# Kernel optimization log

Hardware: AMD Instinct MI355X
Metric: run time of the kernel (lower is better)

Reference implementation:

```python
import jax, jax.numpy as jnp
import numpy as np

NT, NS, NH = 1096, 2048, 16

def setup_inputs() -> dict:
    key = jax.random.key(0)
    ks = jax.random.split(key, 6)
    # precipitation (non-negative) and temperature (can be +/-)
    P = jax.random.uniform(ks[0], (NT, NS), dtype=jnp.float32) * 10.0
    T = jax.random.normal(ks[1], (NT, NS), dtype=jnp.float32) * 10.0
    w_i = jax.random.uniform(ks[2], (NH,), minval=-1.0, maxval=1.0, dtype=jnp.float32)
    w_o = jax.random.uniform(ks[3], (NH,), minval=-1.0, maxval=1.0, dtype=jnp.float32)
    w_l = jax.random.uniform(ks[4], (NH,), minval=-1.0, maxval=1.0, dtype=jnp.float32)  # LinearBucket.w
    w_s = jax.random.uniform(ks[5], (NH,), minval=-1.0, maxval=2.0, dtype=jnp.float32)  # SnowBucket.w
    return dict(P=P, T=T, w_i=w_i, w_o=w_o, w_l=w_l, w_s=w_s)


def reference(P, T, w_i, w_o, w_l, w_s):
    # Time-invariant gate factors (Dropout is identity in eval mode)
    melt_coef = jnp.exp(w_s) + 1.0          # [nh]
    gi = jax.nn.sigmoid(w_i)                # [nh] input gate
    gl = jax.nn.sigmoid(w_l)                # [nh] linear-bucket release fraction
    a = jax.nn.softmax(w_o)                 # [nh] output mixing weights

    ns = P.shape[1]
    nh = w_i.shape[0]
    s0 = jnp.zeros((ns, nh), P.dtype)
    h0 = jnp.zeros((ns, nh), P.dtype)

    def step(carry, pt):
        s, h = carry
        Pk, Tk = pt                          # [ns]
        # SnowBucket (nm=0: melt m = min(potential melt, snow store))
        sm = jax.nn.relu(Tk)[:, None] * melt_coef      # [ns, nh]
        m = jnp.minimum(sm, s)
        sn = s - m + jnp.where(Tk < 0, Pk, 0.0)[:, None]
        x = jnp.where(Tk > 0, Pk, 0.0)[:, None] + m
        # input gate + LinearBucket
        xin = x * gi
        q = (xin + h) * gl
        hn = h - q + xin
        Qk = jnp.sum(q * a, axis=1)                    # [ns]
        return (sn, hn), (Qk, hn, sn)

    _, (Q, H, S) = jax.lax.scan(step, (s0, h0), (P, T))
    return Q, H, S
```

## Files before the change

### kernel.cpp

```cpp
#include <hip/hip_runtime.h>


constexpr int NT  = 1096;
constexpr int NS  = 2048;
constexpr int NH  = 16;
constexpr int NSH = NS * NH;
constexpr int SG  = 4;
constexpr int NC  = 8;
constexpr int L   = NT / NC;
static_assert(NC * L == NT, "");
constexpr int BT  = NC * SG * NH;
constexpr int NXCD = 8;

__device__ __forceinline__ float sigm(float x) { return 1.0f / (1.0f + expf(-x)); }

__global__ __launch_bounds__(BT, 4) void waternet_fused(
    const float* __restrict__ P, const float* __restrict__ T,
    const float* __restrict__ w_i, const float* __restrict__ w_o,
    const float* __restrict__ w_l, const float* __restrict__ w_s,
    float* __restrict__ Q, float* __restrict__ H, float* __restrict__ S)
{
    __shared__ float2 PTs[SG][NT + 2];
    __shared__ float bufA[BT];
    __shared__ float bufB[BT];
    __shared__ float bufC[BT];

    const int nwg = NS / SG;
    const int cpx = nwg / NXCD;
    const int bid = (int)blockIdx.x;
    const int lbid = (bid % NXCD) * cpx + bid / NXCD;

    const int tid  = (int)threadIdx.x;
    const int hh   = tid & (NH - 1);
    const int sl   = (tid >> 4) & (SG - 1);
    const int c    = tid >> 6;
    const int site0 = lbid * SG;

    for (int e = tid; e < SG * NT; e += BT) {
        const int t  = e >> 2;
        const int s2 = e & 3;
        const float p  = P[(size_t)t * NS + site0 + s2];
        const float tt = T[(size_t)t * NS + site0 + s2];
        PTs[s2][t] = make_float2(p, tt);
    }

    const float mc = expf(w_s[hh]) + 1.0f;
    const float gi = sigm(w_i[hh]);
    const float gl = sigm(w_l[hh]);
    const float cl = 1.0f - gl;

    const int t0 = c * L;
    __syncthreads();

    float A = 0.0f, B = -1e38f;
    for (int i = 0; i < L; ++i) {
        const float2 pt = PTs[sl][t0 + i];
        const float tpos = fmaxf(pt.y, 0.0f);
        const float pnn  = (pt.y < 0.0f) ? pt.x : 0.0f;
        const float at   = pnn - tpos * mc;
        A += at;
        B = fmaxf(B + at, pnn);
    }
    bufA[tid] = A;
    bufB[tid] = B;
    __syncthreads();

    if (tid < SG * NH) {
        float s = 0.0f;
        #pragma unroll
        for (int k = 0; k < NC; ++k) {
            const int idx = k * (SG * NH) + tid;
            bufC[idx] = s;
            s = fmaxf(s + bufA[idx], bufB[idx]);
        }
    }
    __syncthreads();

    float s = bufC[tid];
    float hp = 0.0f;
    {
        float* Sp = S + (size_t)t0 * NSH + (size_t)site0 * NH + sl * NH + hh;
        for (int i = 0; i < L; ++i) {
            const float2 pt = PTs[sl][t0 + i];
            const float tpos = fmaxf(pt.y, 0.0f);
            const float pnn  = (pt.y < 0.0f) ? pt.x : 0.0f;
            const float ppp  = (pt.y > 0.0f) ? pt.x : 0.0f;
            const float m    = fminf(tpos * mc, s);
            s = s - m + pnn;
            Sp[(size_t)i * NSH] = s;
            const float xin = (ppp + m) * gi;
            hp = cl * (hp + xin);
        }
    }
    bufA[tid] = hp;
    __syncthreads();

    if (tid < SG * NH) {
        const float clr = 1.0f - sigm(w_l[tid & (NH - 1)]);
        const float clL = powf(clr, (float)L);
        float h = 0.0f;
        #pragma unroll
        for (int k = 0; k < NC; ++k) {
            const int idx = k * (SG * NH) + tid;
            bufB[idx] = h;
            h = clL * h + bufA[idx];
        }
    }
    __syncthreads();

    float mx = -1e30f;
    #pragma unroll
    for (int j = 0; j < NH; ++j) mx = fmaxf(mx, w_o[j]);
    float den = 0.0f;
    #pragma unroll
    for (int j = 0; j < NH; ++j) den += expf(w_o[j] - mx);
    const float aw = expf(w_o[hh] - mx) / den;

    s = bufC[tid];
    float h = bufB[tid];
    {
        float* Hp = H + (size_t)t0 * NSH + (size_t)site0 * NH + sl * NH + hh;
        float* Qp = Q + (size_t)t0 * NS + site0 + sl;
        for (int i = 0; i < L; ++i) {
            const float2 pt = PTs[sl][t0 + i];
            const float tpos = fmaxf(pt.y, 0.0f);
            const float pnn  = (pt.y < 0.0f) ? pt.x : 0.0f;
            const float ppp  = (pt.y > 0.0f) ? pt.x : 0.0f;
            const float m    = fminf(tpos * mc, s);
            s = s - m + pnn;
            const float xin = (ppp + m) * gi;
            const float q   = (xin + h) * gl;
            h = cl * (h + xin);
            Hp[(size_t)i * NSH] = h;
            float qa = q * aw;
            qa += __shfl_xor(qa, 1, 16);
            qa += __shfl_xor(qa, 2, 16);
            qa += __shfl_xor(qa, 4, 16);
            qa += __shfl_xor(qa, 8, 16);
            if (hh == 0) Qp[(size_t)i * NS] = qa;
        }
    }
}

extern "C" void kernel_launch(void* const* d_in, const int* in_sizes, int n_in,
                              void* d_out, int out_size, void* d_ws, size_t ws_size,
                              hipStream_t stream) {
    const float* P   = (const float*)d_in[0];
    const float* T   = (const float*)d_in[1];
    const float* w_i = (const float*)d_in[2];
    const float* w_o = (const float*)d_in[3];
    const float* w_l = (const float*)d_in[4];
    const float* w_s = (const float*)d_in[5];

    float* Q = (float*)d_out;
    float* H = Q + (size_t)NT * NS;
    float* S = H + (size_t)NT * NS * NH;

    waternet_fused<<<NS / SG, BT, 0, stream>>>(P, T, w_i, w_o, w_l, w_s, Q, H, S);
}
```

Baseline: 328.7 us.

## Split time into 16 chunks with two hidden units per thread

Doubles the number of time chunks from 8 to 16 (chunk lengths 69 and 68) and has each thread handle two hidden units, keeping 512 threads per block. This shortens each thread's serial recurrence. The outputs S and H are now stored as float2, the Q reduction needs one fewer shuffle, and P/T are loaded as float4 per timestep. The serial scan across chunks gets twice as many steps, and each thread holds more registers.

```diff
diff --git a/kernel.cpp b/kernel.cpp
--- a/kernel.cpp
+++ b/kernel.cpp
@@ -6,10 +6,10 @@
 constexpr int NH  = 16;
 constexpr int NSH = NS * NH;
 constexpr int SG  = 4;
-constexpr int NC  = 8;
-constexpr int L   = NT / NC;
-static_assert(NC * L == NT, "");
-constexpr int BT  = NC * SG * NH;
+constexpr int NC  = 16;
+constexpr int LA  = 69;
+constexpr int LB  = 68;
+constexpr int BT  = 512;
 constexpr int NXCD = 8;
 
 __device__ __forceinline__ float sigm(float x) { return 1.0f / (1.0f + expf(-x)); }
@@ -21,124 +21,183 @@
     float* __restrict__ Q, float* __restrict__ H, float* __restrict__ S)
 {
     __shared__ float2 PTs[SG][NT + 2];
-    __shared__ float bufA[BT];
-    __shared__ float bufB[BT];
-    __shared__ float bufC[BT];
-
-    const int nwg = NS / SG;
-    const int cpx = nwg / NXCD;
-    const int bid = (int)blockIdx.x;
+    __shared__ float bufA[BT * 2];
+    __shared__ float bufB[BT * 2];
+    __shared__ float bufC[BT * 2];
+
+    const int nwg  = NS / SG;
+    const int cpx  = nwg / NXCD;
+    const int bid  = (int)blockIdx.x;
     const int lbid = (bid % NXCD) * cpx + bid / NXCD;
 
     const int tid  = (int)threadIdx.x;
-    const int hh   = tid & (NH - 1);
-    const int sl   = (tid >> 4) & (SG - 1);
-    const int c    = tid >> 6;
+    const int hh2  = tid & 7;
+    const int sl   = (tid >> 3) & (SG - 1);
+    const int c    = tid >> 5;
     const int site0 = lbid * SG;
 
-    for (int e = tid; e < SG * NT; e += BT) {
-        const int t  = e >> 2;
-        const int s2 = e & 3;
-        const float p  = P[(size_t)t * NS + site0 + s2];
-        const float tt = T[(size_t)t * NS + site0 + s2];
-        PTs[s2][t] = make_float2(p, tt);
-    }
-
-    const float mc = expf(w_s[hh]) + 1.0f;
-    const float gi = sigm(w_i[hh]);
-    const float gl = sigm(w_l[hh]);
-    const float cl = 1.0f - gl;
-
-    const int t0 = c * L;
-    __syncthreads();
-
-    float A = 0.0f, B = -1e38f;
-    for (int i = 0; i < L; ++i) {
-        const float2 pt = PTs[sl][t0 + i];
-        const float tpos = fmaxf(pt.y, 0.0f);
-        const float pnn  = (pt.y < 0.0f) ? pt.x : 0.0f;
-        const float at   = pnn - tpos * mc;
-        A += at;
-        B = fmaxf(B + at, pnn);
-    }
-    bufA[tid] = A;
-    bufB[tid] = B;
+    const int t0  = (c < 8) ? (LA * c) : (LA * 8 + LB * (c - 8));
+    const int len = (c < 8) ? LA : LB;
+
+    for (int t = tid; t < NT; t += BT) {
+        const float4 p4 = *(const float4*)(P + (size_t)t * NS + site0);
+        const float4 t4 = *(const float4*)(T + (size_t)t * NS + site0);
+        PTs[0][t] = make_float2(p4.x, t4.x);
+        PTs[1][t] = make_float2(p4.y, t4.y);
+        PTs[2][t] = make_float2(p4.z, t4.z);
+        PTs[3][t] = make_float2(p4.w, t4.w);
+    }
+
+    float mc[2], gi[2], gl[2], cl[2];
+    #pragma unroll
+    for (int p = 0; p < 2; ++p) {
+        const int hh = hh2 * 2 + p;
+        mc[p] = expf(w_s[hh]) + 1.0f;
+        gi[p] = sigm(w_i[hh]);
+        gl[p] = sigm(w_l[hh]);
+        cl[p] = 1.0f - gl[p];
+    }
+
+    __syncthreads();
+
+    float A[2] = {0.0f, 0.0f}, B[2] = {-1e38f, -1e38f};
+    {
+        const float2* pts = &PTs[sl][t0];
+        auto stepAB = [&](float2 pt) {
+            const float tpos = fmaxf(pt.y, 0.0f);
+            const float pnn  = (pt.y < 0.0f) ? pt.x : 0.0f;
+            #pragma unroll
+            for (int p = 0; p < 2; ++p) {
+                const float at = pnn - tpos * mc[p];
+                A[p] += at;
+                B[p] = fmaxf(B[p] + at, pnn);
+            }
+        };
+        int i = 0;
+        for (; i + 4 <= len; i += 4) {
+            float2 v0 = pts[i], v1 = pts[i+1], v2 = pts[i+2], v3 = pts[i+3];
+            stepAB(v0); stepAB(v1); stepAB(v2); stepAB(v3);
+        }
+        for (; i < len; ++i) stepAB(pts[i]);
+    }
+    bufA[tid * 2]     = A[0];
+    bufA[tid * 2 + 1] = A[1];
+    bufB[tid * 2]     = B[0];
+    bufB[tid * 2 + 1] = B[1];
     __syncthreads();
 
     if (tid < SG * NH) {
+        const int rsl = tid >> 4, rhh = tid & 15;
+        const int sub = rsl * 16 + rhh;
         float s = 0.0f;
         #pragma unroll
         for (int k = 0; k < NC; ++k) {
-            const int idx = k * (SG * NH) + tid;
+            const int idx = k * 64 + sub;
             bufC[idx] = s;
             s = fmaxf(s + bufA[idx], bufB[idx]);
         }
     }
     __syncthreads();
 
-    float s = bufC[tid];
-    float hp = 0.0f;
-    {
-        float* Sp = S + (size_t)t0 * NSH + (size_t)site0 * NH + sl * NH + hh;
-        for (int i = 0; i < L; ++i) {
-            const float2 pt = PTs[sl][t0 + i];
+    float s[2], hp[2] = {0.0f, 0.0f};
+    s[0] = bufC[tid * 2];
+    s[1] = bufC[tid * 2 + 1];
+    {
+        const float2* pts = &PTs[sl][t0];
+        float2* Sp = (float2*)(S + (size_t)t0 * NSH + (size_t)site0 * NH
+                               + sl * NH + hh2 * 2);
+        auto step2 = [&](float2 pt, int i) {
             const float tpos = fmaxf(pt.y, 0.0f);
             const float pnn  = (pt.y < 0.0f) ? pt.x : 0.0f;
             const float ppp  = (pt.y > 0.0f) ? pt.x : 0.0f;
-            const float m    = fminf(tpos * mc, s);
-            s = s - m + pnn;
-            Sp[(size_t)i * NSH] = s;
-            const float xin = (ppp + m) * gi;
-            hp = cl * (hp + xin);
-        }
-    }
-    bufA[tid] = hp;
+            float2 sv;
+            #pragma unroll
+            for (int p = 0; p < 2; ++p) {
+                const float m = fminf(tpos * mc[p], s[p]);
+                s[p] = s[p] - m + pnn;
+                const float xin = (ppp + m) * gi[p];
+                hp[p] = cl[p] * (hp[p] + xin);
+                (p ? sv.y : sv.x) = s[p];
+            }
+            Sp[(size_t)i * (NSH / 2)] = sv;
+        };
+        int i = 0;
+        for (; i + 4 <= len; i += 4) {
+            float2 v0 = pts[i], v1 = pts[i+1], v2 = pts[i+2], v3 = pts[i+3];
+            step2(v0, i); step2(v1, i+1); step2(v2, i+2); step2(v3, i+3);
+        }
+        for (; i < len; ++i) step2(pts[i], i);
+    }
+    bufA[tid * 2]     = hp[0];
+    bufA[tid * 2 + 1] = hp[1];
     __syncthreads();
 
     if (tid < SG * NH) {
-        const float clr = 1.0f - sigm(w_l[tid & (NH - 1)]);
-        const float clL = powf(clr, (float)L);
+        const int rsl = tid >> 4, rhh = tid & 15;
+        const int sub = rsl * 16 + rhh;
+        const float clr = 1.0f - sigm(w_l[rhh]);
+        const float pA = powf(clr, (float)LA);
+        const float pB = powf(clr, (float)LB);
         float h = 0.0f;
         #pragma unroll
         for (int k = 0; k < NC; ++k) {
-            const int idx = k * (SG * NH) + tid;
+            const int idx = k * 64 + sub;
             bufB[idx] = h;
-            h = clL * h + bufA[idx];
-        }
-    }
-    __syncthreads();
-
-    float mx = -1e30f;
-    #pragma unroll
-    for (int j = 0; j < NH; ++j) mx = fmaxf(mx, w_o[j]);
-    float den = 0.0f;
-    #pragma unroll
-    for (int j = 0; j < NH; ++j) den += expf(w_o[j] - mx);
-    const float aw = expf(w_o[hh] - mx) / den;
-
-    s = bufC[tid];
-    float h = bufB[tid];
-    {
-        float* Hp = H + (size_t)t0 * NSH + (size_t)site0 * NH + sl * NH + hh;
+            h = ((k < 8) ? pA : pB) * h + bufA[idx];
+        }
+    }
+    __syncthreads();
+
+    float aw[2];
+    {
+        float mx = -1e30f;
+        #pragma unroll
+        for (int j = 0; j < NH; ++j) mx = fmaxf(mx, w_o[j]);
+        float den = 0.0f;
+        #pragma unroll
+        for (int j = 0; j < NH; ++j) den += expf(w_o[j] - mx);
+        aw[0] = expf(w_o[hh2 * 2]     - mx) / den;
+        aw[1] = expf(w_o[hh2 * 2 + 1] - mx) / den;
+    }
+
+    s[0] = bufC[tid * 2];
+    s[1] = bufC[tid * 2 + 1];
+    float h[2];
+    h[0] = bufB[tid * 2];
+    h[1] = bufB[tid * 2 + 1];
+    {
+        const float2* pts = &PTs[sl][t0];
+        float2* Hp = (float2*)(H + (size_t)t0 * NSH + (size_t)site0 * NH
+                               + sl * NH + hh2 * 2);
         float* Qp = Q + (size_t)t0 * NS + site0 + sl;
-        for (int i = 0; i < L; ++i) {
-            const float2 pt = PTs[sl][t0 + i];
+        auto step3 = [&](float2 pt, int i) {
             const float tpos = fmaxf(pt.y, 0.0f);
             const float pnn  = (pt.y < 0.0f) ? pt.x : 0.0f;
             const float ppp  = (pt.y > 0.0f) ? pt.x : 0.0f;
-            const float m    = fminf(tpos * mc, s);
-            s = s - m + pnn;
-            const float xin = (ppp + m) * gi;
-            const float q   = (xin + h) * gl;
-            h = cl * (h + xin);
-            Hp[(size_t)i * NSH] = h;
-            float qa = q * aw;
-            qa += __shfl_xor(qa, 1, 16);
-            qa += __shfl_xor(qa, 2, 16);
-            qa += __shfl_xor(qa, 4, 16);
-            qa += __shfl_xor(qa, 8, 16);
-            if (hh == 0) Qp[(size_t)i * NS] = qa;
-        }
+            float2 hv;
+            float qa = 0.0f;
+            #pragma unroll
+            for (int p = 0; p < 2; ++p) {
+                const float m = fminf(tpos * mc[p], s[p]);
+                s[p] = s[p] - m + pnn;
+                const float xin = (ppp + m) * gi[p];
+                const float q   = (xin + h[p]) * gl[p];
+                h[p] = cl[p] * (h[p] + xin);
+                (p ? hv.y : hv.x) = h[p];
+                qa += q * aw[p];
+            }
+            Hp[(size_t)i * (NSH / 2)] = hv;
+            qa += __shfl_xor(qa, 1, 8);
+            qa += __shfl_xor(qa, 2, 8);
+            qa += __shfl_xor(qa, 4, 8);
+            if (hh2 == 0) Qp[(size_t)i * NS] = qa;
+        };
+        int i = 0;
+        for (; i + 4 <= len; i += 4) {
+            float2 v0 = pts[i], v1 = pts[i+1], v2 = pts[i+2], v3 = pts[i+3];
+            step3(v0, i); step3(v1, i+1); step3(v2, i+2); step3(v3, i+3);
+        }
+        for (; i < len; ++i) step3(pts[i], i);
     }
 }
 
```

Measured after the change: 316.6 us. 3.7% less time.
